# Performance work log

Hardware: AMD Instinct MI355X
Metric: run time of the kernel (lower is better)

The kernel has to match this reference:

```python
import jax, jax.numpy as jnp
import numpy as np

B, N, D = 4, 4096, 1024
H, S, R = 16, 256, 2           # heads, segment size, dilation rate
DH = D // H
LN_EPS = 1e-5


def _hilbert_perm(n_side):
    # perm[d] = linear index (y*side + x) of the d-th point on the Hilbert curve
    def d2xy(n, d):
        x = y = 0
        t = d
        s = 1
        while s < n:
            rx = 1 & (t // 2)
            ry = 1 & (t ^ rx)
            if ry == 0:
                if rx == 1:
                    x = s - 1 - x
                    y = s - 1 - y
                x, y = y, x
            x += s * rx
            y += s * ry
            t //= 4
            s *= 2
        return x, y
    perm = np.empty(n_side * n_side, dtype=np.int32)
    for d in range(n_side * n_side):
        xx, yy = d2xy(n_side, d)
        perm[d] = yy * n_side + xx
    return perm


def setup_inputs() -> dict:
    key = jax.random.key(0)
    ks = jax.random.split(key, 8)
    sc = 0.02
    return {
        "x": jax.random.normal(ks[0], (B, N, D), jnp.float32),
        "ln1_g": jnp.ones((D,), jnp.float32),
        "ln1_b": jnp.zeros((D,), jnp.float32),
        "w_qkv": jax.random.normal(ks[1], (D, 3 * D), jnp.float32) * sc,
        "b_qkv": jnp.zeros((3 * D,), jnp.float32),
        "w_o": jax.random.normal(ks[2], (D, D), jnp.float32) * sc,
        "b_o": jnp.zeros((D,), jnp.float32),
        "ln2_g": jnp.ones((D,), jnp.float32),
        "ln2_b": jnp.zeros((D,), jnp.float32),
        "w1": jax.random.normal(ks[3], (D, 4 * D), jnp.float32) * sc,
        "b1": jnp.zeros((4 * D,), jnp.float32),
        "w2": jax.random.normal(ks[4], (4 * D, D), jnp.float32) * sc,
        "b2": jnp.zeros((D,), jnp.float32),
        "hilbert_perm": jnp.asarray(_hilbert_perm(int(np.sqrt(N)))),
    }


def _layernorm(x, g, b):
    mu = jnp.mean(x, axis=-1, keepdims=True)
    var = jnp.mean(jnp.square(x - mu), axis=-1, keepdims=True)
    return (x - mu) * jax.lax.rsqrt(var + LN_EPS) * g + b


def _hilbert_dilated_attention(x, w_qkv, b_qkv, w_o, b_o, perm):
    b, n, d = x.shape
    nseg, sr = n // S, S // R
    xp = jnp.take(x, perm, axis=1)                    # Hilbert reorder
    qkv = xp @ w_qkv + b_qkv                          # [b,n,3d]
    q, k, v = jnp.split(qkv, 3, axis=-1)
    def seg(t):
        return t.reshape(b, nseg, S, H, DH)
    q, k, v = seg(q), seg(k), seg(v)
    # per-head dilation offset: head h attends positions (h % R) :: R in each segment
    offs = jnp.arange(H, dtype=jnp.int32) % R                        # [H]
    idx = offs[None, :] + R * jnp.arange(sr, dtype=jnp.int32)[:, None]  # [sr,H]
    idx_g = idx[None, None, :, :, None]                              # [1,1,sr,H,1]
    qd = jnp.take_along_axis(q, idx_g, axis=2)        # [b,nseg,sr,H,dh]
    kd = jnp.take_along_axis(k, idx_g, axis=2)
    vd = jnp.take_along_axis(v, idx_g, axis=2)
    scores = jnp.einsum('bgqhd,bgkhd->bghqk', qd, kd) / jnp.sqrt(jnp.asarray(DH, x.dtype))
    attn = jax.nn.softmax(scores, axis=-1)
    od = jnp.einsum('bghqk,bgkhd->bgqhd', attn, vd)   # [b,nseg,sr,H,dh]
    # scatter back into full segments; uncovered (head,pos) slots stay zero
    out = jnp.zeros((b, nseg, S, H, DH), x.dtype)
    out = out.at[:, :, idx, jnp.arange(H)[None, :], :].set(od)
    out = out.reshape(b, n, d) @ w_o + b_o
    inv = jnp.argsort(perm)
    return jnp.take(out, inv, axis=1)                 # inverse Hilbert reorder


def reference(x, ln1_g, ln1_b, w_qkv, b_qkv, w_o, b_o, ln2_g, ln2_b, w1, b1, w2, b2, hilbert_perm):
    h = _layernorm(x, ln1_g, ln1_b)
    h = _hilbert_dilated_attention(h, w_qkv, b_qkv, w_o, b_o, hilbert_perm)
    x = x + h
    h = _layernorm(x, ln2_g, ln2_b)
    h = jax.nn.gelu(h @ w1 + b1, approximate=False) @ w2 + b2
    return x + h
```

## Files before the change

kernel.cpp:

```cpp
#include <hip/hip_runtime.h>
#include <hip/hip_fp8.h>

typedef short bf16x8 __attribute__((ext_vector_type(8)));
typedef float f32x4 __attribute__((ext_vector_type(4)));
typedef unsigned short u16;
typedef unsigned char u8;

#define GLDS16(g, l) __builtin_amdgcn_global_load_lds( \
    (const __attribute__((address_space(1))) void*)(g), \
    (__attribute__((address_space(3))) void*)(l), 16, 0, 0)

#define DSR_(dst, p) asm volatile("ds_read_b128 %0, %1" \
    : "=v"(dst) : "v"((const __attribute__((address_space(3))) void*)(p)))
#define DSR64_(dst, p) asm volatile("ds_read_b64 %0, %1" \
    : "=v"(dst) : "v"((const __attribute__((address_space(3))) void*)(p)))

__device__ __forceinline__ u16 f2b(float f) {
  unsigned u = __float_as_uint(f);
  u += 0x7fffu + ((u >> 16) & 1u);
  return (u16)(u >> 16);
}
__device__ __forceinline__ float b2f(u16 b) {
  return __uint_as_float(((unsigned)b) << 16);
}
__device__ __forceinline__ u8 f2e4(float v) {
  __hip_fp8_e4m3 t(v);
  return *reinterpret_cast<u8*>(&t);
}

__global__ __launch_bounds__(256)
void transpose_bf16(const float* __restrict__ w, u16* __restrict__ wt, int K, int N) {
  __shared__ float tile[32][33];
  const int n0 = blockIdx.x * 32, k0 = blockIdx.y * 32;
  const int tx = threadIdx.x & 31, ty = threadIdx.x >> 5;
#pragma unroll
  for (int i = 0; i < 4; ++i)
    tile[ty + i * 8][tx] = w[(size_t)(k0 + ty + i * 8) * N + n0 + tx];
  __syncthreads();
#pragma unroll
  for (int i = 0; i < 4; ++i)
    wt[(size_t)(n0 + ty + i * 8) * K + k0 + tx] = f2b(tile[tx][ty + i * 8]);
}

__global__ __launch_bounds__(256)
void transpose_fp8(const float* __restrict__ w, u8* __restrict__ wt, int K, int N) {
  __shared__ float tile[32][33];
  const int n0 = blockIdx.x * 32, k0 = blockIdx.y * 32;
  const int tx = threadIdx.x & 31, ty = threadIdx.x >> 5;
#pragma unroll
  for (int i = 0; i < 4; ++i)
    tile[ty + i * 8][tx] = w[(size_t)(k0 + ty + i * 8) * N + n0 + tx];
  __syncthreads();
#pragma unroll
  for (int i = 0; i < 4; ++i)
    wt[(size_t)(n0 + ty + i * 8) * K + k0 + tx] = f2e4(16.f * tile[tx][ty + i * 8]);
}

__global__ __launch_bounds__(256)
void transpose_qkv_pack(const float* __restrict__ w, u16* __restrict__ wp) {
  __shared__ float tile[32][33];
  const int n0 = blockIdx.x * 32, k0 = blockIdx.y * 32;
  const int tx = threadIdx.x & 31, ty = threadIdx.x >> 5;
#pragma unroll
  for (int i = 0; i < 4; ++i)
    tile[ty + i * 8][tx] = w[(size_t)(k0 + ty + i * 8) * 3072 + n0 + tx];
  __syncthreads();
#pragma unroll
  for (int i = 0; i < 4; ++i) {
    const int col = n0 + ty + i * 8;
    const int q = (col >> 6) & 1;
    const int np = (col >> 10) * 512 + ((col >> 7) & 7) * 64 + (col & 63);
    wp[(size_t)q * (1536 * 1024) + (size_t)np * 1024 + k0 + tx] = f2b(tile[tx][ty + i * 8]);
  }
}

__global__ __launch_bounds__(256)
void transpose_wo_pack(const float* __restrict__ w, u16* __restrict__ wp) {
  __shared__ float tile[32][33];
  const int n0 = blockIdx.x * 32, k0 = blockIdx.y * 32;
  const int tx = threadIdx.x & 31, ty = threadIdx.x >> 5;
#pragma unroll
  for (int i = 0; i < 4; ++i)
    tile[ty + i * 8][tx] = w[(size_t)(k0 + ty + i * 8) * 1024 + n0 + tx];
  __syncthreads();
#pragma unroll
  for (int i = 0; i < 4; ++i) {
    const int n = n0 + ty + i * 8;
    const int k = k0 + tx;
    const int q = (k >> 6) & 1;
    const int kp = (k >> 7) * 64 + (k & 63);
    wp[(size_t)q * (1024 * 512) + (size_t)n * 512 + kp] = f2b(tile[tx][ty + i * 8]);
  }
}

template <int BF16IN, int OUT8>
__global__ __launch_bounds__(256)
void ln_rows(const void* __restrict__ srcv, const float* __restrict__ gam,
             const float* __restrict__ bet, const int* __restrict__ perm,
             void* __restrict__ dstv) {
  const int orow = blockIdx.x;
  const int b = orow >> 12, j = orow & 4095;
  const int srow = perm ? ((b << 12) + perm[j]) : orow;
  float4 v;
  if (BF16IN) {
    const uint2 raw = ((const uint2*)((const u16*)srcv + (size_t)srow * 1024))[threadIdx.x];
    v.x = b2f((u16)(raw.x & 0xffff)); v.y = b2f((u16)(raw.x >> 16));
    v.z = b2f((u16)(raw.y & 0xffff)); v.w = b2f((u16)(raw.y >> 16));
  } else {
    v = ((const float4*)((const float*)srcv + (size_t)srow * 1024))[threadIdx.x];
  }
  float s = v.x + v.y + v.z + v.w;
  float s2 = v.x * v.x + v.y * v.y + v.z * v.z + v.w * v.w;
#pragma unroll
  for (int d = 1; d < 64; d <<= 1) { s += __shfl_xor(s, d); s2 += __shfl_xor(s2, d); }
  __shared__ float rs[4], rs2[4];
  const int wave = threadIdx.x >> 6, lane = threadIdx.x & 63;
  if (lane == 0) { rs[wave] = s; rs2[wave] = s2; }
  __syncthreads();
  s = rs[0] + rs[1] + rs[2] + rs[3];
  s2 = rs2[0] + rs2[1] + rs2[2] + rs2[3];
  const float mu = s * (1.f / 1024.f);
  const float var = s2 * (1.f / 1024.f) - mu * mu;
  const float rstd = rsqrtf(var + 1e-5f);
  const int c = threadIdx.x * 4;
  const float4 gg = *(const float4*)(gam + c);
  const float4 bb = *(const float4*)(bet + c);
  const float o0 = (v.x - mu) * rstd * gg.x + bb.x;
  const float o1 = (v.y - mu) * rstd * gg.y + bb.y;
  const float o2 = (v.z - mu) * rstd * gg.z + bb.z;
  const float o3 = (v.w - mu) * rstd * gg.w + bb.w;
  if (OUT8) {
    const unsigned p = (unsigned)f2e4(4.f * o0) | ((unsigned)f2e4(4.f * o1) << 8) |
                       ((unsigned)f2e4(4.f * o2) << 16) | ((unsigned)f2e4(4.f * o3) << 24);
    *(unsigned*)((u8*)dstv + (size_t)orow * 1024 + c) = p;
  } else {
    const unsigned lo = (unsigned)f2b(o0) | ((unsigned)f2b(o1) << 16);
    const unsigned hi = (unsigned)f2b(o2) | ((unsigned)f2b(o3) << 16);
    *(uint2*)((u16*)dstv + (size_t)orow * 1024 + c) = make_uint2(lo, hi);
  }
}

template <int EPI, int PAR>
__global__ __launch_bounds__(512, 2)
void gemm256(const u16* __restrict__ A, const u16* __restrict__ Bt,
             const float* __restrict__ bias, void* __restrict__ Cout,
             const void* __restrict__ resid, const int* __restrict__ perm,
             int M, int Nn, int K, int aRS,
             long aParOff, long bParOff, long cParOff) {
  __shared__ u16 sm[65536];
  char* const smc = (char*)sm;
  const int tid = threadIdx.x;
  const int w = tid >> 6, lane = tid & 63;
  const int lr = lane & 15, lg = lane >> 4;
  const int wm = w >> 2, wn = w & 3;

  int wg = blockIdx.x;
  int par = 0;
  if (PAR) { par = wg & 1; wg >>= 1; }
  const int x = wg & 7, l = wg >> 3;
  const int band = (M >> 8) >> 3;
  const int mm = l % band, nn = l / band;
  const int m0 = (x * band + mm) << 8;
  const int n0 = nn << 8;

  const int srow = tid >> 3;
  const int scol = ((tid & 7) ^ (srow & 7)) << 3;
  const size_t aSrc = (size_t)(m0 + srow) * aRS + (PAR ? (size_t)par * aParOff : 0) + scol;
  const size_t bSrc = (size_t)(n0 + srow) * K + (PAR ? (size_t)par * bParOff : 0) + scol;

  const int slot0 = (lg ^ (lr & 7)) << 4;
  const int aRow = (wm * 128 + lr) * 128;
  const int bRow = 32768 + (wn * 64 + lr) * 128;

  const int NT = K >> 6;

#define STAGE_(d, mat, h, k0) do { \
    const size_t rs_ = (mat) ? (size_t)K : (size_t)aRS; \
    const u16* gp = ((mat) ? Bt : A) + ((mat) ? bSrc : aSrc) + (size_t)(h) * 128 * rs_ + (k0); \
    char* lp = smc + (d) * 65536 + (mat) * 32768 + (h) * 16384 + w * 1024; \
    GLDS16(gp, lp); GLDS16(gp + 64 * rs_, lp + 8192); } while (0)

  bf16x8 aLo[8], aHi[8], bLo[4], bHi[4];

#define R_ALO(P) do { _Pragma("unroll") for (int mf = 0; mf < 4; ++mf) \
    _Pragma("unroll") for (int kk = 0; kk < 2; ++kk) \
      DSR_(aLo[mf * 2 + kk], (P) + aRow + mf * 2048 + (slot0 ^ (kk << 6))); } while (0)
#define R_AHI(P) do { _Pragma("unroll") for (int mf = 0; mf < 4; ++mf) \
    _Pragma("unroll") for (int kk = 0; kk < 2; ++kk) \
      DSR_(aHi[mf * 2 + kk], (P) + aRow + (4 + mf) * 2048 + (slot0 ^ (kk << 6))); } while (0)
#define R_BLO(P) do { _Pragma("unroll") for (int nf = 0; nf < 2; ++nf) \
    _Pragma("unroll") for (int kk = 0; kk < 2; ++kk) \
      DSR_(bLo[nf * 2 + kk], (P) + bRow + nf * 2048 + (slot0 ^ (kk << 6))); } while (0)
#define R_BHI(P) do { _Pragma("unroll") for (int nf = 0; nf < 2; ++nf) \
    _Pragma("unroll") for (int kk = 0; kk < 2; ++kk) \
      DSR_(bHi[nf * 2 + kk], (P) + bRow + (2 + nf) * 2048 + (slot0 ^ (kk << 6))); } while (0)

#define QUAD_(AARR, BARR, MB, NB) do { _Pragma("unroll") for (int mf = 0; mf < 4; ++mf) \
    _Pragma("unroll") for (int nf = 0; nf < 2; ++nf) \
    _Pragma("unroll") for (int kk = 0; kk < 2; ++kk) \
      acc[(MB) * 4 + mf][(NB) * 2 + nf] = __builtin_amdgcn_mfma_f32_16x16x32_bf16( \
          AARR[mf * 2 + kk], BARR[nf * 2 + kk], acc[(MB) * 4 + mf][(NB) * 2 + nf], 0, 0, 0); } while (0)

#define LGKM0SB_() do { asm volatile("s_waitcnt lgkmcnt(0)" ::: "memory"); \
                        __builtin_amdgcn_sched_barrier(0); } while (0)

  STAGE_(0, 1, 0, 0); STAGE_(0, 1, 1, 0); STAGE_(0, 0, 0, 0); STAGE_(0, 0, 1, 0);
  if (NT > 1) {
    STAGE_(1, 1, 0, 64); STAGE_(1, 1, 1, 64); STAGE_(1, 0, 0, 64); STAGE_(1, 0, 1, 64);
    asm volatile("s_waitcnt vmcnt(8)" ::: "memory");
  } else {
    asm volatile("s_waitcnt vmcnt(0)" ::: "memory");
  }
  __builtin_amdgcn_s_barrier();

  f32x4 acc[8][4] = {};

  for (int t = 0; t < NT; ++t) {
    const int c = t & 1;
    const char* cbuf = smc + c * 65536;
    const int k2 = (t + 2) << 6;

    R_ALO(cbuf); R_BLO(cbuf);
    LGKM0SB_();
    __builtin_amdgcn_s_setprio(1);
    QUAD_(aLo, bLo, 0, 0);
    __builtin_amdgcn_s_setprio(0);
    R_BHI(cbuf);
    LGKM0SB_();
    __builtin_amdgcn_s_setprio(1);
    QUAD_(aLo, bHi, 0, 1);
    __builtin_amdgcn_s_setprio(0);
    __builtin_amdgcn_s_barrier();
    if (t + 2 < NT) { STAGE_(c, 1, 0, k2); STAGE_(c, 1, 1, k2); }
    R_AHI(cbuf);
    LGKM0SB_();
    __builtin_amdgcn_s_setprio(1);
    QUAD_(aHi, bLo, 1, 0);
    __builtin_amdgcn_s_setprio(0);
    __builtin_amdgcn_s_barrier();
    if (t + 2 < NT) { STAGE_(c, 0, 0, k2); STAGE_(c, 0, 1, k2); }
    __builtin_amdgcn_s_setprio(1);
    QUAD_(aHi, bHi, 1, 1);
    __builtin_amdgcn_s_setprio(0);
    if (t + 2 < NT) asm volatile("s_waitcnt vmcnt(8)" ::: "memory");
    else            asm volatile("s_waitcnt vmcnt(0)" ::: "memory");
    __builtin_amdgcn_s_barrier();
  }
#undef STAGE_
#undef R_ALO
#undef R_AHI
#undef R_BLO
#undef R_BHI
#undef QUAD_
#undef LGKM0SB_

#pragma unroll
  for (int mf = 0; mf < 8; ++mf) {
#pragma unroll
    for (int nf = 0; nf < 4; ++nf) {
      const int col = n0 + wn * 64 + nf * 16 + lr;
      float bia;
      if (PAR && EPI == 0) {
        const int s = col >> 9, hh2 = (col >> 6) & 7, d = col & 63;
        bia = bias[s * 1024 + hh2 * 128 + par * 64 + d];
      } else {
        bia = bias[col];
      }
#pragma unroll
      for (int r = 0; r < 4; ++r) {
        const int row = m0 + wm * 128 + mf * 16 + lg * 4 + r;
        float v = acc[mf][nf][r] + bia;
        if (EPI == 0) {
          ((u16*)Cout)[(PAR ? (size_t)par * cParOff : 0) + (size_t)row * Nn + col] = f2b(v);
        } else if (EPI == 2) {
          const int orig = PAR ? (2 * row + par) : row;
          const int b2 = orig >> 12, jj = orig & 4095;
          const size_t di = ((size_t)((b2 << 12) + perm[jj])) * 1024 + col;
          ((u16*)Cout)[di] = f2b(((const float*)resid)[di] + v);
        } else {
          const size_t di = (size_t)row * 1024 + col;
          ((float*)Cout)[di] = b2f(((const u16*)resid)[di]) + v;
        }
      }
    }
  }
}

__global__ __launch_bounds__(512, 2)
void gemm_f8(const u8* __restrict__ A, const u8* __restrict__ Bt,
             const float* __restrict__ bias, u16* __restrict__ Cout,
             int M, int Nn, int K) {
  __shared__ u16 sm[65536];
  char* const smc = (char*)sm;
  const int tid = threadIdx.x;
  const int w = tid >> 6, lane = tid & 63;
  const int lr = lane & 15, lg = lane >> 4;
  const int wm = w >> 2, wn = w & 3;

  const int wg = blockIdx.x;
  const int x = wg & 7, l = wg >> 3;
  const int band = (M >> 8) >> 3;
  const int mm = l % band, nn = l / band;
  const int m0 = (x * band + mm) << 8;
  const int n0 = nn << 8;

  const int srow8 = tid >> 3;
  const int scol8 = ((tid & 7) ^ ((srow8 >> 1) & 7)) << 4;
  const size_t aSrc = (size_t)(m0 + srow8) * K + scol8;
  const size_t bSrc = (size_t)(n0 + srow8) * K + scol8;

  const int aRowB = (wm * 128 + lr) * 128;
  const int bRowB = 32768 + (wn * 64 + lr) * 128;
  int slotf[4];
#pragma unroll
  for (int kk = 0; kk < 4; ++kk) slotf[kk] = ((kk * 4 + lg) ^ (lr & 14)) << 3;

  const int NT = K >> 7;

#define STAGE8_(d, mat, h, k0) do { \
    const u8* gp = ((mat) ? Bt : A) + ((mat) ? bSrc : aSrc) + (size_t)(h) * 128 * K + (k0); \
    char* lp = smc + (d) * 65536 + (mat) * 32768 + (h) * 16384 + w * 1024; \
    GLDS16(gp, lp); GLDS16(gp + (size_t)64 * K, lp + 8192); } while (0)

  long aLo[16], aHi[16], bLo[8], bHi[8];

#define R8_ALO(P) do { _Pragma("unroll") for (int mf = 0; mf < 4; ++mf) \
    _Pragma("unroll") for (int kk = 0; kk < 4; ++kk) \
      DSR64_(aLo[mf * 4 + kk], (P) + aRowB + mf * 2048 + slotf[kk]); } while (0)
#define R8_AHI(P) do { _Pragma("unroll") for (int mf = 0; mf < 4; ++mf) \
    _Pragma("unroll") for (int kk = 0; kk < 4; ++kk) \
      DSR64_(aHi[mf * 4 + kk], (P) + aRowB + (4 + mf) * 2048 + slotf[kk]); } while (0)
#define R8_BLO(P) do { _Pragma("unroll") for (int nf = 0; nf < 2; ++nf) \
    _Pragma("unroll") for (int kk = 0; kk < 4; ++kk) \
      DSR64_(bLo[nf * 4 + kk], (P) + bRowB + nf * 2048 + slotf[kk]); } while (0)
#define R8_BHI(P) do { _Pragma("unroll") for (int nf = 0; nf < 2; ++nf) \
    _Pragma("unroll") for (int kk = 0; kk < 4; ++kk) \
      DSR64_(bHi[nf * 4 + kk], (P) + bRowB + (2 + nf) * 2048 + slotf[kk]); } while (0)

#define QUAD8_(AARR, BARR, MB, NB) do { _Pragma("unroll") for (int kk = 0; kk < 4; ++kk) \
    _Pragma("unroll") for (int mf = 0; mf < 4; ++mf) \
    _Pragma("unroll") for (int nf = 0; nf < 2; ++nf) \
      acc[(MB) * 4 + mf][(NB) * 2 + nf] = __builtin_amdgcn_mfma_f32_16x16x32_fp8_fp8( \
          AARR[mf * 4 + kk], BARR[nf * 4 + kk], acc[(MB) * 4 + mf][(NB) * 2 + nf], 0, 0, 0); } while (0)

#define LGKM0SB_() do { asm volatile("s_waitcnt lgkmcnt(0)" ::: "memory"); \
                        __builtin_amdgcn_sched_barrier(0); } while (0)

  STAGE8_(0, 1, 0, 0); STAGE8_(0, 1, 1, 0); STAGE8_(0, 0, 0, 0); STAGE8_(0, 0, 1, 0);
  if (NT > 1) {
    STAGE8_(1, 1, 0, 128); STAGE8_(1, 1, 1, 128); STAGE8_(1, 0, 0, 128); STAGE8_(1, 0, 1, 128);
    asm volatile("s_waitcnt vmcnt(8)" ::: "memory");
  } else {
    asm volatile("s_waitcnt vmcnt(0)" ::: "memory");
  }
  __builtin_amdgcn_s_barrier();

  f32x4 acc[8][4] = {};

  for (int t = 0; t < NT; ++t) {
    const int c = t & 1;
    const char* cbuf = smc + c * 65536;
    const int k2 = (t + 2) << 7;

    R8_ALO(cbuf); R8_BLO(cbuf);
    LGKM0SB_();
    __builtin_amdgcn_s_setprio(1);
    QUAD8_(aLo, bLo, 0, 0);
    __builtin_amdgcn_s_setprio(0);
    R8_BHI(cbuf);
    LGKM0SB_();
    __builtin_amdgcn_s_setprio(1);
    QUAD8_(aLo, bHi, 0, 1);
    __builtin_amdgcn_s_setprio(0);
    __builtin_amdgcn_s_barrier();
    if (t + 2 < NT) { STAGE8_(c, 1, 0, k2); STAGE8_(c, 1, 1, k2); }
    R8_AHI(cbuf);
    LGKM0SB_();
    __builtin_amdgcn_s_setprio(1);
    QUAD8_(aHi, bLo, 1, 0);
    __builtin_amdgcn_s_setprio(0);
    __builtin_amdgcn_s_barrier();
    if (t + 2 < NT) { STAGE8_(c, 0, 0, k2); STAGE8_(c, 0, 1, k2); }
    __builtin_amdgcn_s_setprio(1);
    QUAD8_(aHi, bHi, 1, 1);
    __builtin_amdgcn_s_setprio(0);
    if (t + 2 < NT) asm volatile("s_waitcnt vmcnt(8)" ::: "memory");
    else            asm volatile("s_waitcnt vmcnt(0)" ::: "memory");
    __builtin_amdgcn_s_barrier();
  }
#undef STAGE8_
#undef R8_ALO
#undef R8_AHI
#undef R8_BLO
#undef R8_BHI
#undef QUAD8_
#undef LGKM0SB_

#pragma unroll
  for (int mf = 0; mf < 8; ++mf) {
#pragma unroll
    for (int nf = 0; nf < 4; ++nf) {
      const int col = n0 + wn * 64 + nf * 16 + lr;
      const float bia = bias[col];
#pragma unroll
      for (int r = 0; r < 4; ++r) {
        const int row = m0 + wm * 128 + mf * 16 + lg * 4 + r;
        float v = acc[mf][nf][r] * 0.015625f + bia;
        v = 0.5f * v * (1.f + erff(v * 0.70710678118654752f));
        Cout[(size_t)row * Nn + col] = f2b(v);
      }
    }
  }
}

__global__ __launch_bounds__(256, 2)
void attn_kernel(const u16* __restrict__ qkvp, u16* __restrict__ op) {
  const int blk = blockIdx.x;
  const int h = blk & 15, g = (blk >> 4) & 15, b = blk >> 8;
  const int tid = threadIdx.x, wave = tid >> 6, lane = tid & 63;
  const int lr = lane & 15, lg = lane >> 4;
  const int par = h & 1, hh = h >> 1;

  __shared__ u16 lQ[128 * 64];
  __shared__ u16 lK[128 * 64];
  __shared__ u16 lVt[64 * 128];
  __shared__ u16 lP[4][32 * 128];

  const u16* qp = qkvp + (size_t)par * (8192 * 1536);
  u16* opb = op + (size_t)par * (8192 * 512);
  const int rbase = (b << 11) + (g << 7);

#pragma unroll
  for (int i = 0; i < 4; ++i) {
    const int ou = i * 4096 + wave * 1024;
    const int o = ou + lane * 16;
    const int j = o >> 7, cb = o & 127;
    const u16* gq = qp + (size_t)(rbase + j) * 1536 + hh * 64 + (cb >> 1);
    GLDS16(gq, (char*)lQ + ou);
    GLDS16(gq + 512, (char*)lK + ou);
  }
#pragma unroll
  for (int i = 0; i < 4; ++i) {
    const int c = tid + i * 256;
    const int j = c >> 3, dc = c & 7;
    const uint4 vv = *(const uint4*)(qp + (size_t)(rbase + j) * 1536 + 1024 + hh * 64 + dc * 8);
    const u16* pv = (const u16*)&vv;
#pragma unroll
    for (int e = 0; e < 8; ++e) lVt[(dc * 8 + e) * 128 + j] = pv[e];
  }
  __syncthreads();

  f32x4 sacc[2][8] = {};
#pragma unroll
  for (int kk = 0; kk < 2; ++kk) {
    bf16x8 aq[2], bk[8];
#pragma unroll
    for (int mf = 0; mf < 2; ++mf)
      aq[mf] = *(const bf16x8*)&lQ[(wave * 32 + mf * 16 + lr) * 64 + kk * 32 + lg * 8];
#pragma unroll
    for (int nf = 0; nf < 8; ++nf)
      bk[nf] = *(const bf16x8*)&lK[(nf * 16 + lr) * 64 + kk * 32 + lg * 8];
#pragma unroll
    for (int mf = 0; mf < 2; ++mf)
#pragma unroll
      for (int nf = 0; nf < 8; ++nf)
        sacc[mf][nf] = __builtin_amdgcn_mfma_f32_16x16x32_bf16(aq[mf], bk[nf], sacc[mf][nf], 0, 0, 0);
  }

#pragma unroll
  for (int mf = 0; mf < 2; ++mf) {
#pragma unroll
    for (int r = 0; r < 4; ++r) {
      float mx = -3e38f;
#pragma unroll
      for (int nf = 0; nf < 8; ++nf) mx = fmaxf(mx, sacc[mf][nf][r]);
#pragma unroll
      for (int d = 1; d < 16; d <<= 1) mx = fmaxf(mx, __shfl_xor(mx, d));
      float pv[8];
      float sum = 0.f;
#pragma unroll
      for (int nf = 0; nf < 8; ++nf) {
        pv[nf] = __expf((sacc[mf][nf][r] - mx) * 0.125f);
        sum += pv[nf];
      }
#pragma unroll
      for (int d = 1; d < 16; d <<= 1) sum += __shfl_xor(sum, d);
      const float inv = 1.f / sum;
      const int rrow = mf * 16 + lg * 4 + r;
#pragma unroll
      for (int nf = 0; nf < 8; ++nf)
        lP[wave][rrow * 128 + nf * 16 + lr] = f2b(pv[nf] * inv);
    }
  }
  __syncthreads();

  f32x4 oacc[2][4] = {};
#pragma unroll
  for (int kk = 0; kk < 4; ++kk) {
    bf16x8 ap[2], bv[4];
#pragma unroll
    for (int mf = 0; mf < 2; ++mf)
      ap[mf] = *(const bf16x8*)&lP[wave][(mf * 16 + lr) * 128 + kk * 32 + lg * 8];
#pragma unroll
    for (int nf = 0; nf < 4; ++nf)
      bv[nf] = *(const bf16x8*)&lVt[(nf * 16 + lr) * 128 + kk * 32 + lg * 8];
#pragma unroll
    for (int mf = 0; mf < 2; ++mf)
#pragma unroll
      for (int nf = 0; nf < 4; ++nf)
        oacc[mf][nf] = __builtin_amdgcn_mfma_f32_16x16x32_bf16(ap[mf], bv[nf], oacc[mf][nf], 0, 0, 0);
  }

  u16* obase = opb + (size_t)rbase * 512 + hh * 64;
#pragma unroll
  for (int mf = 0; mf < 2; ++mf)
#pragma unroll
    for (int nf = 0; nf < 4; ++nf)
#pragma unroll
      for (int r = 0; r < 4; ++r) {
        const int jq = wave * 32 + mf * 16 + lg * 4 + r;
        obase[(size_t)jq * 512 + nf * 16 + lr] = f2b(oacc[mf][nf][r]);
      }
}

extern "C" void kernel_launch(void* const* d_in, const int* in_sizes, int n_in,
                              void* d_out, int out_size, void* d_ws, size_t ws_size,
                              hipStream_t stream) {
  const float* x    = (const float*)d_in[0];
  const float* ln1g = (const float*)d_in[1];
  const float* ln1b = (const float*)d_in[2];
  const float* wqkv = (const float*)d_in[3];
  const float* bqkv = (const float*)d_in[4];
  const float* wo   = (const float*)d_in[5];
  const float* bo   = (const float*)d_in[6];
  const float* ln2g = (const float*)d_in[7];
  const float* ln2b = (const float*)d_in[8];
  const float* w1   = (const float*)d_in[9];
  const float* b1   = (const float*)d_in[10];
  const float* w2   = (const float*)d_in[11];
  const float* b2   = (const float*)d_in[12];
  const int*   perm = (const int*)d_in[13];
  float* out = (float*)d_out;
  char* ws = (char*)d_ws;

  u16*  r0    = (u16*)ws;
  u8*   r8    = (u8*)ws;
  u16*  qkvp  = (u16*)(ws + (32ull << 20));
  u16*  op    = (u16*)(ws + (80ull << 20));
  u16*  a1    = (u16*)(ws + (32ull << 20));
  u16*  x2    = (u16*)(ws + (160ull << 20));
  u16*  wqkvP = (u16*)(ws + (224ull << 20));
  u16*  woP   = (u16*)(ws + (230ull << 20));
  u8*   w1T8  = (u8*)(ws + (232ull << 20));
  u16*  w2T   = (u16*)(ws + (240ull << 20));

  transpose_qkv_pack<<<dim3(96, 32), 256, 0, stream>>>(wqkv, wqkvP);
  transpose_wo_pack<<<dim3(32, 32), 256, 0, stream>>>(wo, woP);
  transpose_fp8<<<dim3(4096 / 32, 1024 / 32), 256, 0, stream>>>(w1, w1T8, 1024, 4096);
  transpose_bf16<<<dim3(1024 / 32, 4096 / 32), 256, 0, stream>>>(w2, w2T, 4096, 1024);

  ln_rows<0, 0><<<16384, 256, 0, stream>>>(x, ln1g, ln1b, perm, r0);
  gemm256<0, 1><<<384, 512, 0, stream>>>(r0, wqkvP, bqkv, qkvp, nullptr, nullptr,
                                         8192, 1536, 1024, 2048,
                                         1024L, 1536L * 1024, 8192L * 1536);
  attn_kernel<<<1024, 256, 0, stream>>>(qkvp, op);
  gemm256<2, 1><<<256, 512, 0, stream>>>(op, woP, bo, x2, x, perm,
                                         8192, 1024, 512, 512,
                                         8192L * 512, 1024L * 512, 0);
  ln_rows<1, 1><<<16384, 256, 0, stream>>>(x2, ln2g, ln2b, nullptr, r8);
  gemm_f8<<<1024, 512, 0, stream>>>(r8, w1T8, b1, a1, 16384, 4096, 1024);
  gemm256<3, 0><<<256, 512, 0, stream>>>(a1, w2T, b2, out, x2, nullptr,
                                         16384, 1024, 4096, 4096, 0, 0, 0);
}
```

Baseline: 489.9 us.

## Add dedicated 256x128 BK32 GEMM for FFN down-projection with higher occupancy

```diff
diff --git a/kernel.cpp b/kernel.cpp
--- a/kernel.cpp
+++ b/kernel.cpp
@@ -286,6 +286,97 @@
   }
 }
 
+__global__ __launch_bounds__(512, 4)
+void gemm_bk32(const u16* __restrict__ A, const u16* __restrict__ Bt,
+               const float* __restrict__ bias, float* __restrict__ Cout,
+               const u16* __restrict__ resid, int M, int Nn, int K) {
+  __shared__ u16 sm[24576];
+  char* const smc = (char*)sm;
+  const int tid = threadIdx.x;
+  const int w = tid >> 6, lane = tid & 63;
+  const int lr = lane & 15, lg = lane >> 4;
+  const int wm = w >> 2, wn = w & 3;
+
+  const int wg = blockIdx.x;
+  const int x = wg & 7, l = wg >> 3;
+  const int mm = l & 7, nn = l >> 3;
+  const int m0 = ((x << 3) + mm) << 8;
+  const int n0 = nn << 7;
+
+  const int sr = lane >> 2, sj = lane & 3;
+  const int sc = ((sj ^ ((sr >> 1) & 3)) << 3);
+  const int sw = (lg ^ ((lr >> 1) & 3)) << 4;
+  const int aRowB = (wm * 128 + lr) * 64;
+  const int bRowB = 16384 + (wn * 32 + lr) * 64;
+
+  const int NT = K >> 5;
+
+#define STAGEA_(d, i, k0) do { \
+    const int rr = w * 32 + (i) * 16 + sr; \
+    GLDS16(A + (size_t)(m0 + rr) * K + (k0) + sc, \
+           smc + (d) * 24576 + w * 2048 + (i) * 1024); } while (0)
+#define STAGEB_(d, k0) do { \
+    const int rr = w * 16 + sr; \
+    GLDS16(Bt + (size_t)(n0 + rr) * K + (k0) + sc, \
+           smc + (d) * 24576 + 16384 + w * 1024); } while (0)
+#define STAGET_(d, k0) do { STAGEA_(d, 0, k0); STAGEA_(d, 1, k0); STAGEB_(d, k0); } while (0)
+
+  bf16x8 a[8], b[2];
+
+#define R_T(P) do { _Pragma("unroll") for (int mf = 0; mf < 8; ++mf) \
+      DSR_(a[mf], (P) + aRowB + mf * 1024 + sw); \
+    _Pragma("unroll") for (int nf = 0; nf < 2; ++nf) \
+      DSR_(b[nf], (P) + bRowB + nf * 1024 + sw); } while (0)
+
+#define LGKM0SB_() do { asm volatile("s_waitcnt lgkmcnt(0)" ::: "memory"); \
+                        __builtin_amdgcn_sched_barrier(0); } while (0)
+
+  STAGET_(0, 0);
+  if (NT > 1) { STAGET_(1, 32); asm volatile("s_waitcnt vmcnt(3)" ::: "memory"); }
+  else        { asm volatile("s_waitcnt vmcnt(0)" ::: "memory"); }
+  __builtin_amdgcn_s_barrier();
+
+  f32x4 acc[8][2] = {};
+
+  for (int t = 0; t < NT; ++t) {
+    const int c = t & 1;
+    R_T(smc + c * 24576);
+    LGKM0SB_();
+    __builtin_amdgcn_s_setprio(1);
+#pragma unroll
+    for (int mf = 0; mf < 8; ++mf)
+#pragma unroll
+      for (int nf = 0; nf < 2; ++nf)
+        acc[mf][nf] = __builtin_amdgcn_mfma_f32_16x16x32_bf16(a[mf], b[nf], acc[mf][nf], 0, 0, 0);
+    __builtin_amdgcn_s_setprio(0);
+    __builtin_amdgcn_s_barrier();
+    if (t + 2 < NT) STAGET_(c, (t + 2) << 5);
+    if (t + 2 < NT) asm volatile("s_waitcnt vmcnt(3)" ::: "memory");
+    else            asm volatile("s_waitcnt vmcnt(0)" ::: "memory");
+    __builtin_amdgcn_s_barrier();
+  }
+#undef STAGEA_
+#undef STAGEB_
+#undef STAGET_
+#undef R_T
+#undef LGKM0SB_
+
+#pragma unroll
+  for (int mf = 0; mf < 8; ++mf) {
+#pragma unroll
+    for (int nf = 0; nf < 2; ++nf) {
+      const int col = n0 + wn * 32 + nf * 16 + lr;
+      const float bia = bias[col];
+#pragma unroll
+      for (int r = 0; r < 4; ++r) {
+        const int row = m0 + wm * 128 + mf * 16 + lg * 4 + r;
+        const size_t di = (size_t)row * 1024 + col;
+        Cout[di] = b2f(resid[di]) + acc[mf][nf][r] + bia;
+      }
+    }
+  }
+}
+
 __global__ __launch_bounds__(512, 2)
 void gemm_f8(const u8* __restrict__ A, const u8* __restrict__ Bt,
              const float* __restrict__ bias, u16* __restrict__ Cout,
@@ -569,6 +660,6 @@
                                          8192L * 512, 1024L * 512, 0);
   ln_rows<1, 1><<<16384, 256, 0, stream>>>(x2, ln2g, ln2b, nullptr, r8);
   gemm_f8<<<1024, 512, 0, stream>>>(r8, w1T8, b1, a1, 16384, 4096, 1024);
-  gemm256<3, 0><<<256, 512, 0, stream>>>(a1, w2T, b2, out, x2, nullptr,
-                                         16384, 1024, 4096, 4096, 0, 0, 0);
-}
+  gemm_bk32<<<512, 512, 0, stream>>>(a1, w2T, b2, out, x2,
+                                     16384, 1024, 4096);
+}
```

After: 514.7 us. +5.1%, slower.
